# Kernel tuning notes

Measured on AMD Instinct MI355X. Metric: run time of the kernel, lower is better.

## Reference

```python
import jax, jax.numpy as jnp
import numpy as np

N = 1_000_000
NG = 128                 # n_grid
DX = 1.0 / NG
DT = 1e-4
P_VOL = (DX * 0.5) ** 2
P_RHO = 1.0
GRAVITY = 9.8
HID = 16


def setup_inputs() -> dict:
    key = jax.random.key(0)
    ks = jax.random.split(key, 14)
    x = 0.1 + 0.8 * jax.random.uniform(ks[0], (N, 2), dtype=jnp.float32)
    v = 0.1 * jax.random.normal(ks[1], (N, 2), dtype=jnp.float32)
    C = 0.01 * jax.random.normal(ks[2], (N, 2, 2), dtype=jnp.float32)
    F = jnp.eye(2, dtype=jnp.float32)[None] + 0.01 * jax.random.normal(ks[3], (N, 2, 2), dtype=jnp.float32)
    material = jax.random.randint(ks[4], (N,), 0, 3, dtype=jnp.int32)
    Jp = jnp.ones((N, 1), dtype=jnp.float32)
    E = jnp.full((1,), 1000.0, dtype=jnp.float32)
    nu = jnp.full((1,), 0.2, dtype=jnp.float32)
    # PsiModel2d MLP params: Linear(2,16) -> Linear(16,16) -> Linear(16,16) -> Linear(16,1)
    s = 0.3
    W1 = s * jax.random.normal(ks[5], (HID, 2), dtype=jnp.float32)
    b1 = jnp.zeros((HID,), dtype=jnp.float32)
    W2 = s * jax.random.normal(ks[6], (HID, HID), dtype=jnp.float32)
    b2 = jnp.zeros((HID,), dtype=jnp.float32)
    W3 = s * jax.random.normal(ks[7], (HID, HID), dtype=jnp.float32)
    b3 = jnp.zeros((HID,), dtype=jnp.float32)
    W4 = s * jax.random.normal(ks[8], (1, HID), dtype=jnp.float32)
    b4 = jnp.zeros((1,), dtype=jnp.float32)
    return dict(x=x, v=v, C=C, F=F, material=material, Jp=Jp, E=E, nu=nu,
                W1=W1, b1=b1, W2=W2, b2=b2, W3=W3, b3=b3, W4=W4, b4=b4)


def _psi_sum(F, W1, b1, W2, b2, W3, b3, W4, b4):
    # PsiModel2d, input_type='eigen': Psi(sigma_1, sigma_2) of C = F^T F
    Cm = jnp.einsum('nki,nkj->nij', F, F)
    tr_C = Cm[:, 0, 0] + Cm[:, 1, 1]
    det_C = Cm[:, 0, 0] * Cm[:, 1, 1] - Cm[:, 0, 1] * Cm[:, 1, 0]
    delta = jnp.sqrt(jnp.maximum(tr_C ** 2 - 4.0 * det_C, 1e-8))
    feat = jnp.stack([0.5 * (tr_C + delta), 0.5 * (tr_C - delta)], axis=1)  # [N,2]
    h = jax.nn.relu(feat @ W1.T + b1)
    h = jax.nn.relu(h @ W2.T + b2)
    h = jax.nn.relu(h @ W3.T + b3)
    return (h @ W4.T + b4).sum()


def reference(x, v, C, F, material, Jp, E, nu, W1, b1, W2, b2, W3, b3, W4, b4):
    inv_dx = float(NG)
    p_mass = P_VOL * P_RHO
    n = x.shape[0]

    base = jnp.floor(x * inv_dx - 0.5).astype(jnp.int32)   # [N,2]
    fx = x * inv_dx - base.astype(x.dtype)                  # [N,2]
    # quadratic B-spline weights, [3,N,2]
    w = jnp.stack([0.5 * (1.5 - fx) ** 2,
                   0.75 - (fx - 1.0) ** 2,
                   0.5 * (fx - 0.5) ** 2], axis=0)

    F_new = F + DT * jnp.einsum('nij,njk->nik', C, F)
    # stress = d(sum Psi)/dF  (learned energy)
    stress = jax.grad(_psi_sum)(F_new, W1, b1, W2, b2, W3, b3, W4, b4)
    stress = (-DT * P_VOL * 4.0 * inv_dx ** 2) * stress
    affine = stress + p_mass * C                            # [N,2,2]

    v_add = p_mass * v - jnp.einsum('nij,nj->ni', affine, x)  # [N,2]
    vals = jnp.concatenate([v_add, affine.reshape(n, 4),
                            jnp.full((n, 1), p_mass, x.dtype)], axis=1)  # [N,7]

    # P2G: scatter-add over 3x3 stencil into flattened grid
    grid = jnp.zeros((NG * NG, 7), x.dtype)
    for i in range(3):
        for j in range(3):
            wt = w[i, :, 0] * w[j, :, 1]                    # [N]
            idx = (base[:, 0] + i) * NG + (base[:, 1] + j)  # [N]
            grid = grid.at[idx].add(wt[:, None] * vals)
    grid = grid.reshape(NG, NG, 7)
    grid_v = grid[..., :2]
    grid_affine = grid[..., 2:6].reshape(NG, NG, 2, 2)
    grid_m = grid[..., 6]

    gx = jnp.stack(jnp.meshgrid(jnp.arange(NG), jnp.arange(NG), indexing='ij'),
                   axis=-1).astype(x.dtype) * DX            # [NG,NG,2]
    grid_v = grid_v + jnp.einsum('xyij,xyj->xyi', grid_affine, gx)
    nonempty = grid_m > 0
    grid_v = jnp.where(nonempty[..., None],
                       grid_v / jnp.where(nonempty, grid_m, 1.0)[..., None],
                       grid_v)
    grid_v = grid_v.at[:, :, 1].add(-DT * GRAVITY)
    # boundary conditions
    grid_v = grid_v.at[:3, :, 0].set(jnp.maximum(grid_v[:3, :, 0], 0.0))
    grid_v = grid_v.at[-3:, :, 0].set(jnp.minimum(grid_v[-3:, :, 0], 0.0))
    grid_v = grid_v.at[:, :3, 1].set(jnp.maximum(grid_v[:, :3, 1], 0.0))
    grid_v = grid_v.at[:, -3:, 1].set(jnp.minimum(grid_v[:, -3:, 1], 0.0))

    # G2P: gather v and v (x) grid_x outer product over 3x3 stencil
    grid_C = grid_v[..., :, None] * gx[..., None, :]        # [NG,NG,2,2]
    gvals = jnp.concatenate([grid_v, grid_C.reshape(NG, NG, 4)], axis=-1)  # [NG,NG,6]
    acc = jnp.zeros((n, 6), x.dtype)
    for i in range(3):
        for j in range(3):
            wt = w[i, :, 0] * w[j, :, 1]
            acc = acc + wt[:, None] * gvals[base[:, 0] + i, base[:, 1] + j]
    new_v = acc[:, :2]
    new_C = acc[:, 2:].reshape(n, 2, 2)
    new_C = (4.0 * inv_dx ** 2) * (new_C - new_v[:, :, None] * x[:, None, :])

    return (x + DT * v, new_v, new_C, F_new, material, Jp)
```

## Files before the change

### kernel.cpp

```cpp
#include <hip/hip_runtime.h>
#include <math.h>

constexpr int   NGc    = 128;
constexpr int   NCELL  = NGc * NGc;
constexpr int   NBIN   = 128 * 128;
constexpr float DTc    = 1e-4f;
constexpr float DXc    = 1.0f / 128.0f;
constexpr float INV_DX = 128.0f;
constexpr float P_VOLc = (DXc * 0.5f) * (DXc * 0.5f);
constexpr float P_MASSc = P_VOLc * 1.0f;
constexpr float GRAV   = 9.8f;
constexpr float STRESS_COEF = -DTc * P_VOLc * 4.0f * INV_DX * INV_DX;

constexpr int KEY_SHIFT = 18;
constexpr unsigned KEY_MASK = (1u << KEY_SHIFT) - 1u;

constexpr int S1_PPT = 4;
constexpr int S1_BLK = 1024;

__global__ __launch_bounds__(1024) void bin_kernel(
    const float2* __restrict__ x, unsigned* __restrict__ key,
    unsigned* __restrict__ gcnt, int n)
{
    __shared__ unsigned hist[NBIN];
#pragma unroll
    for (int j = 0; j < NBIN / S1_BLK; j++)
        hist[threadIdx.x + j * S1_BLK] = 0;
    __syncthreads();

    int base_i = blockIdx.x * (S1_BLK * S1_PPT);
    unsigned t_arr[S1_PPT], r_arr[S1_PPT];
#pragma unroll
    for (int k = 0; k < S1_PPT; k++) {
        int i = base_i + k * S1_BLK + threadIdx.x;
        unsigned t = 0, r = 0;
        if (i < n) {
            float2 xi = x[i];
            int bx = (int)floorf(xi.x * INV_DX - 0.5f);
            int by = (int)floorf(xi.y * INV_DX - 0.5f);
            t = (unsigned)(bx * 128 + by);
            r = atomicAdd(&hist[t], 1u);
        }
        t_arr[k] = t; r_arr[k] = r;
    }
    __syncthreads();

#pragma unroll
    for (int j = 0; j < NBIN / S1_BLK; j++) {
        int b = threadIdx.x + j * S1_BLK;
        unsigned c = hist[b];
        __syncthreads();
        hist[b] = c ? atomicAdd(&gcnt[b], c) : 0u;
        __syncthreads();
    }

#pragma unroll
    for (int k = 0; k < S1_PPT; k++) {
        int i = base_i + k * S1_BLK + threadIdx.x;
        if (i < n)
            key[i] = (t_arr[k] << KEY_SHIFT) | (hist[t_arr[k]] + r_arr[k]);
    }
}

__global__ __launch_bounds__(1024) void scan_kernel(
    const unsigned* __restrict__ gcnt, unsigned* __restrict__ binoff)
{
    __shared__ unsigned s[1024];
    int t = threadIdx.x;
    unsigned v[16];
    unsigned p = 0;
#pragma unroll
    for (int k = 0; k < 16; k++) { v[k] = gcnt[16 * t + k]; p += v[k]; }
    s[t] = p;
    __syncthreads();
    for (int d = 1; d < 1024; d <<= 1) {
        unsigned add = (t >= d) ? s[t - d] : 0u;
        __syncthreads();
        s[t] += add;
        __syncthreads();
    }
    unsigned base = s[t] - p;
#pragma unroll
    for (int k = 0; k < 16; k++) { binoff[16 * t + k] = base; base += v[k]; }
    if (t == 1023) binoff[NBIN] = s[1023];
}

#define RL(v, l) __int_as_float(__builtin_amdgcn_readlane(__float_as_int(v), (l)))

__global__ __launch_bounds__(256) void stagea_kernel(
    const float2* __restrict__ x, const float2* __restrict__ v,
    const float4* __restrict__ C, const float4* __restrict__ F,
    const float* __restrict__ W1, const float* __restrict__ b1,
    const float* __restrict__ W2, const float* __restrict__ b2,
    const float* __restrict__ W3, const float* __restrict__ b3,
    const float* __restrict__ W4,
    const unsigned* __restrict__ key, const unsigned* __restrict__ binoff,
    float4* __restrict__ recs, float4* __restrict__ out_F, int n)
{
    const int lane = threadIdx.x & 63;

    float w2r[4], w3r[4];
#pragma unroll
    for (int r = 0; r < 4; r++) {
        w2r[r] = W2[r * 64 + lane];
        w3r[r] = W3[r * 64 + lane];
    }
    float wa = (lane < 32) ? W1[lane]
             : ((lane < 48) ? b1[lane - 32] : W4[lane - 48]);
    float wb = (lane < 16) ? b2[lane]
             : ((lane < 32) ? b3[lane - 16] : 0.0f);

    int i = blockIdx.x * 256 + threadIdx.x;
    if (i >= n) return;

    float2 xi = x[i];
    float2 vi = v[i];
    float4 Ci = C[i];
    float4 Fi = F[i];

    float Fn00 = Fi.x + DTc * (Ci.x * Fi.x + Ci.y * Fi.z);
    float Fn01 = Fi.y + DTc * (Ci.x * Fi.y + Ci.y * Fi.w);
    float Fn10 = Fi.z + DTc * (Ci.z * Fi.x + Ci.w * Fi.z);
    float Fn11 = Fi.w + DTc * (Ci.z * Fi.y + Ci.w * Fi.w);

    out_F[i] = make_float4(Fn00, Fn01, Fn10, Fn11);

    float Cm00 = Fn00 * Fn00 + Fn10 * Fn10;
    float Cm01 = Fn00 * Fn01 + Fn10 * Fn11;
    float Cm11 = Fn01 * Fn01 + Fn11 * Fn11;

    float tr  = Cm00 + Cm11;
    float det = Cm00 * Cm11 - Cm01 * Cm01;
    float g   = tr * tr - 4.0f * det;
    float gate = (g > 1e-8f) ? 1.0f : 0.0f;
    float delta = sqrtf(fmaxf(g, 1e-8f));
    float feat0 = 0.5f * (tr + delta);
    float feat1 = 0.5f * (tr - delta);

    float h1[16];
#pragma unroll
    for (int j = 0; j < 16; j++) {
        float a = RL(wa, 2 * j) * feat0 + RL(wa, 2 * j + 1) * feat1 + RL(wa, 32 + j);
        h1[j] = fmaxf(a, 0.0f);
    }

    float h2[16];
#pragma unroll
    for (int j = 0; j < 16; j++) {
        float a0 = RL(wb, j), a1 = 0.0f, a2 = 0.0f, a3 = 0.0f;
#pragma unroll
        for (int k = 0; k < 16; k += 4) {
            a0 += RL(w2r[(16 * j + k + 0) >> 6], (16 * j + k + 0) & 63) * h1[k + 0];
            a1 += RL(w2r[(16 * j + k + 1) >> 6], (16 * j + k + 1) & 63) * h1[k + 1];
            a2 += RL(w2r[(16 * j + k + 2) >> 6], (16 * j + k + 2) & 63) * h1[k + 2];
            a3 += RL(w2r[(16 * j + k + 3) >> 6], (16 * j + k + 3) & 63) * h1[k + 3];
        }
        h2[j] = fmaxf((a0 + a1) + (a2 + a3), 0.0f);
    }

    float dh3[16];
#pragma unroll
    for (int j = 0; j < 16; j++) {
        float a0 = RL(wb, 16 + j), a1 = 0.0f, a2 = 0.0f, a3 = 0.0f;
#pragma unroll
        for (int k = 0; k < 16; k += 4) {
            a0 += RL(w3r[(16 * j + k + 0) >> 6], (16 * j + k + 0) & 63) * h2[k + 0];
            a1 += RL(w3r[(16 * j + k + 1) >> 6], (16 * j + k + 1) & 63) * h2[k + 1];
            a2 += RL(w3r[(16 * j + k + 2) >> 6], (16 * j + k + 2) & 63) * h2[k + 2];
            a3 += RL(w3r[(16 * j + k + 3) >> 6], (16 * j + k + 3) & 63) * h2[k + 3];
        }
        float a = (a0 + a1) + (a2 + a3);
        dh3[j] = (a > 0.0f) ? RL(wa, 48 + j) : 0.0f;
    }

    float dh2[16];
#pragma unroll
    for (int kk = 0; kk < 16; kk++) {
        float a0 = 0.0f, a1 = 0.0f, a2 = 0.0f, a3 = 0.0f;
#pragma unroll
        for (int j = 0; j < 16; j += 4) {
            a0 += RL(w3r[(16 * (j + 0) + kk) >> 6], (16 * (j + 0) + kk) & 63) * dh3[j + 0];
            a1 += RL(w3r[(16 * (j + 1) + kk) >> 6], (16 * (j + 1) + kk) & 63) * dh3[j + 1];
            a2 += RL(w3r[(16 * (j + 2) + kk) >> 6], (16 * (j + 2) + kk) & 63) * dh3[j + 2];
            a3 += RL(w3r[(16 * (j + 3) + kk) >> 6], (16 * (j + 3) + kk) & 63) * dh3[j + 3];
        }
        float a = (a0 + a1) + (a2 + a3);
        dh2[kk] = (h2[kk] > 0.0f) ? a : 0.0f;
    }

    float dfeat0 = 0.0f, dfeat1 = 0.0f;
#pragma unroll
    for (int kk = 0; kk < 16; kk++) {
        float a0 = 0.0f, a1 = 0.0f, a2 = 0.0f, a3 = 0.0f;
#pragma unroll
        for (int j = 0; j < 16; j += 4) {
            a0 += RL(w2r[(16 * (j + 0) + kk) >> 6], (16 * (j + 0) + kk) & 63) * dh2[j + 0];
            a1 += RL(w2r[(16 * (j + 1) + kk) >> 6], (16 * (j + 1) + kk) & 63) * dh2[j + 1];
            a2 += RL(w2r[(16 * (j + 2) + kk) >> 6], (16 * (j + 2) + kk) & 63) * dh2[j + 2];
            a3 += RL(w2r[(16 * (j + 3) + kk) >> 6], (16 * (j + 3) + kk) & 63) * dh2[j + 3];
        }
        float a = (a0 + a1) + (a2 + a3);
        float dh1k = (h1[kk] > 0.0f) ? a : 0.0f;
        dfeat0 += RL(wa, 2 * kk) * dh1k;
        dfeat1 += RL(wa, 2 * kk + 1) * dh1k;
    }

    float half_sum  = 0.5f * (dfeat0 + dfeat1);
    float half_diff = 0.5f * (dfeat0 - dfeat1);
    float inv_delta = 1.0f / delta;
    float dtr  = half_sum + half_diff * tr * inv_delta * gate;
    float ddet = half_diff * (-2.0f) * inv_delta * gate;

    float S00 = 2.0f * (dtr + ddet * Cm11);
    float S11 = 2.0f * (dtr + ddet * Cm00);
    float S01 = -2.0f * ddet * Cm01;

    float dF00 = Fn00 * S00 + Fn01 * S01;
    float dF01 = Fn00 * S01 + Fn01 * S11;
    float dF10 = Fn10 * S00 + Fn11 * S01;
    float dF11 = Fn10 * S01 + Fn11 * S11;

    float a00 = STRESS_COEF * dF00 + P_MASSc * Ci.x;
    float a01 = STRESS_COEF * dF01 + P_MASSc * Ci.y;
    float a10 = STRESS_COEF * dF10 + P_MASSc * Ci.z;
    float a11 = STRESS_COEF * dF11 + P_MASSc * Ci.w;

    unsigned k = key[i];
    unsigned pos = binoff[k >> KEY_SHIFT] + (k & KEY_MASK);

    recs[2 * (size_t)pos]     = make_float4(xi.x, xi.y, a00, a01);
    recs[2 * (size_t)pos + 1] = make_float4(a10, a11, P_MASSc * vi.x, P_MASSc * vi.y);
}

__global__ __launch_bounds__(256) void grid_gather_kernel(
    const float4* __restrict__ recs, const unsigned* __restrict__ binoff,
    float2* __restrict__ gv)
{
    int wid  = threadIdx.x >> 6;
    int lane = threadIdx.x & 63;
    int node = blockIdx.x * 4 + wid;
    int gi = node >> 7;
    int gj = node & 127;

    const float gxx = (float)gi * DXc;
    const float gxy = (float)gj * DXc;

    float accx = 0.0f, accy = 0.0f, accm = 0.0f;

    int j0 = max(gj - 2, 0);

#pragma unroll
    for (int r = 0; r < 3; r++) {
        int bx = gi - 2 + r;
        if (bx < 0 || bx > 127) continue;
        int lo = (int)binoff[bx * 128 + j0];
        int hi = (int)binoff[bx * 128 + gj + 1];
        for (int k = lo + lane; k < hi; k += 64) {
            float4 r0 = recs[2 * (size_t)k];
            float4 r1 = recs[2 * (size_t)k + 1];

            float py = r0.y * INV_DX;
            int   by = (int)floorf(py - 0.5f);
            int   jj = gj - by;

            float fy = py - (float)by;
            float fx = r0.x * INV_DX - (float)bx;

            float wx;
            if (r == 0)      wx = 0.5f * (fx - 0.5f) * (fx - 0.5f);
            else if (r == 1) wx = 0.75f - (fx - 1.0f) * (fx - 1.0f);
            else             wx = 0.5f * (1.5f - fx) * (1.5f - fx);

            float wy0 = 0.5f * (1.5f - fy) * (1.5f - fy);
            float wy1 = 0.75f - (fy - 1.0f) * (fy - 1.0f);
            float wy2 = 0.5f * (fy - 0.5f) * (fy - 0.5f);
            float wy = (jj == 0) ? wy0 : ((jj == 1) ? wy1 : wy2);

            float wt = wx * wy;
            float dxp = gxx - r0.x;
            float dyp = gxy - r0.y;
            accx += wt * (r1.z + r0.z * dxp + r0.w * dyp);
            accy += wt * (r1.w + r1.x * dxp + r1.y * dyp);
            accm += wt * P_MASSc;
        }
    }

#pragma unroll
    for (int off = 32; off >= 1; off >>= 1) {
        accx += __shfl_xor(accx, off, 64);
        accy += __shfl_xor(accy, off, 64);
        accm += __shfl_xor(accm, off, 64);
    }

    if (lane == 0) {
        float vx = accx, vy = accy;
        if (accm > 0.0f) {
            float inv_m = 1.0f / accm;
            vx *= inv_m;
            vy *= inv_m;
        }
        vy -= DTc * GRAV;
        if (gi < 3)        vx = fmaxf(vx, 0.0f);
        if (gi >= NGc - 3) vx = fminf(vx, 0.0f);
        if (gj < 3)        vy = fmaxf(vy, 0.0f);
        if (gj >= NGc - 3) vy = fminf(vy, 0.0f);
        gv[node] = make_float2(vx, vy);
    }
}

__global__ __launch_bounds__(256) void g2p_kernel(
    const float2* __restrict__ x, const float2* __restrict__ v,
    const int* __restrict__ material, const float* __restrict__ Jp,
    const float2* __restrict__ gv,
    float2* __restrict__ out_x, float2* __restrict__ out_v,
    float4* __restrict__ out_C,
    float* __restrict__ out_mat, float* __restrict__ out_Jp, int n)
{
    int i = blockIdx.x * 256 + threadIdx.x;
    if (i >= n) return;

    float2 xi = x[i];
    float2 vi = v[i];

    float px = xi.x * INV_DX, py = xi.y * INV_DX;
    int   bx = (int)floorf(px - 0.5f);
    int   by = (int)floorf(py - 0.5f);
    float fx = px - (float)bx;
    float fy = py - (float)by;
    float wxs[3] = {0.5f * (1.5f - fx) * (1.5f - fx),
                    0.75f - (fx - 1.0f) * (fx - 1.0f),
                    0.5f * (fx - 0.5f) * (fx - 0.5f)};
    float wys[3] = {0.5f * (1.5f - fy) * (1.5f - fy),
                    0.75f - (fy - 1.0f) * (fy - 1.0f),
                    0.5f * (fy - 0.5f) * (fy - 0.5f)};

    float accvx = 0.0f, accvy = 0.0f;
    float accC00 = 0.0f, accC01 = 0.0f, accC10 = 0.0f, accC11 = 0.0f;

#pragma unroll
    for (int ii = 0; ii < 3; ii++) {
        float gxx = (float)(bx + ii) * DXc;
#pragma unroll
        for (int jj = 0; jj < 3; jj++) {
            float wt = wxs[ii] * wys[jj];
            float2 gvn = gv[(bx + ii) * NGc + (by + jj)];
            float gxy = (float)(by + jj) * DXc;
            accvx  += wt * gvn.x;
            accvy  += wt * gvn.y;
            accC00 += wt * gvn.x * gxx;
            accC01 += wt * gvn.x * gxy;
            accC10 += wt * gvn.y * gxx;
            accC11 += wt * gvn.y * gxy;
        }
    }

    const float k4 = 4.0f * INV_DX * INV_DX;
    out_x[i]   = make_float2(xi.x + DTc * vi.x, xi.y + DTc * vi.y);
    out_v[i]   = make_float2(accvx, accvy);
    out_C[i]   = make_float4(k4 * (accC00 - accvx * xi.x),
                             k4 * (accC01 - accvx * xi.y),
                             k4 * (accC10 - accvy * xi.x),
                             k4 * (accC11 - accvy * xi.y));
    out_mat[i] = (float)material[i];
    out_Jp[i]  = Jp[i];
}

extern "C" void kernel_launch(void* const* d_in, const int* in_sizes, int n_in,
                              void* d_out, int out_size, void* d_ws, size_t ws_size,
                              hipStream_t stream)
{
    const float2* x  = (const float2*)d_in[0];
    const float2* v  = (const float2*)d_in[1];
    const float4* C  = (const float4*)d_in[2];
    const float4* F  = (const float4*)d_in[3];
    const int* material = (const int*)d_in[4];
    const float* Jp  = (const float*)d_in[5];
    const float* W1  = (const float*)d_in[8];
    const float* b1  = (const float*)d_in[9];
    const float* W2  = (const float*)d_in[10];
    const float* b2  = (const float*)d_in[11];
    const float* W3  = (const float*)d_in[12];
    const float* b3  = (const float*)d_in[13];
    const float* W4  = (const float*)d_in[14];

    const int n = in_sizes[0] / 2;

    float2* gv = (float2*)d_ws;

    float* out = (float*)d_out;
    float2* out_x   = (float2*)out;
    float2* out_v   = (float2*)(out + 2 * (size_t)n);
    float4* out_C   = (float4*)(out + 4 * (size_t)n);
    float4* out_F   = (float4*)(out + 8 * (size_t)n);
    float*  out_mat = out + 12 * (size_t)n;
    float*  out_Jp  = out + 13 * (size_t)n;

    float4*   recs   = (float4*)out;
    unsigned* key    = (unsigned*)out_mat;
    unsigned* gcnt   = (unsigned*)(out + 13 * (size_t)n);
    unsigned* binoff = gcnt + NBIN;

    hipMemsetAsync(gcnt, 0, NBIN * sizeof(unsigned), stream);

    int s1_blocks = (n + S1_BLK * S1_PPT - 1) / (S1_BLK * S1_PPT);
    int blocks    = (n + 255) / 256;
    bin_kernel<<<s1_blocks, S1_BLK, 0, stream>>>(x, key, gcnt, n);
    scan_kernel<<<1, 1024, 0, stream>>>(gcnt, binoff);
    stagea_kernel<<<blocks, 256, 0, stream>>>(x, v, C, F, W1, b1, W2, b2, W3, b3, W4,
                                              key, binoff, recs, out_F, n);
    grid_gather_kernel<<<NCELL / 4, 256, 0, stream>>>(recs, binoff, gv);
    g2p_kernel<<<blocks, 256, 0, stream>>>(x, v, material, Jp, gv,
                                           out_x, out_v, out_C, out_mat, out_Jp, n);
}
```

Before: 254.0 us.

## Replace global atomic bin offsets with per-block histograms and column scan

The binning kernel now writes each block's local histogram to a per-block count table instead of atomically adding into a global counter array. A new column-scan kernel turns these into per-block exclusive offsets and per-bin totals, and stage A adds the per-block offset when scattering records. Blocks are also made larger, cutting the grid to about 58 blocks, which removes global atomics, the memset and the second key pass. The price is a serial per-bin scan over blocks, an extra kernel launch, another indirect load in stage A, and low occupancy in the binning pass.

```diff
diff --git a/kernel.cpp b/kernel.cpp
--- a/kernel.cpp
+++ b/kernel.cpp
@@ -15,12 +15,13 @@
 constexpr int KEY_SHIFT = 18;
 constexpr unsigned KEY_MASK = (1u << KEY_SHIFT) - 1u;
 
-constexpr int S1_PPT = 4;
-constexpr int S1_BLK = 1024;
+constexpr int S1_PPT   = 17;
+constexpr int S1_BLK   = 1024;
+constexpr int S1_CHUNK = S1_BLK * S1_PPT;
 
 __global__ __launch_bounds__(1024) void bin_kernel(
     const float2* __restrict__ x, unsigned* __restrict__ key,
-    unsigned* __restrict__ gcnt, int n)
+    unsigned* __restrict__ counts, int n)
 {
     __shared__ unsigned hist[NBIN];
 #pragma unroll
@@ -28,49 +29,53 @@
         hist[threadIdx.x + j * S1_BLK] = 0;
     __syncthreads();
 
-    int base_i = blockIdx.x * (S1_BLK * S1_PPT);
-    unsigned t_arr[S1_PPT], r_arr[S1_PPT];
+    int base_i = blockIdx.x * S1_CHUNK;
 #pragma unroll
     for (int k = 0; k < S1_PPT; k++) {
         int i = base_i + k * S1_BLK + threadIdx.x;
-        unsigned t = 0, r = 0;
         if (i < n) {
             float2 xi = x[i];
             int bx = (int)floorf(xi.x * INV_DX - 0.5f);
             int by = (int)floorf(xi.y * INV_DX - 0.5f);
-            t = (unsigned)(bx * 128 + by);
-            r = atomicAdd(&hist[t], 1u);
-        }
-        t_arr[k] = t; r_arr[k] = r;
+            unsigned t = (unsigned)(bx * 128 + by);
+            unsigned r = atomicAdd(&hist[t], 1u);
+            key[i] = (t << KEY_SHIFT) | r;
+        }
     }
     __syncthreads();
 
+    unsigned* row = counts + (size_t)blockIdx.x * NBIN;
 #pragma unroll
     for (int j = 0; j < NBIN / S1_BLK; j++) {
         int b = threadIdx.x + j * S1_BLK;
-        unsigned c = hist[b];
-        __syncthreads();
-        hist[b] = c ? atomicAdd(&gcnt[b], c) : 0u;
-        __syncthreads();
-    }
-
-#pragma unroll
-    for (int k = 0; k < S1_PPT; k++) {
-        int i = base_i + k * S1_BLK + threadIdx.x;
-        if (i < n)
-            key[i] = (t_arr[k] << KEY_SHIFT) | (hist[t_arr[k]] + r_arr[k]);
-    }
+        row[b] = hist[b];
+    }
+}
+
+__global__ __launch_bounds__(256) void scan_blocks_kernel(
+    unsigned* __restrict__ counts, unsigned* __restrict__ bintotal, int nblk)
+{
+    int bin = blockIdx.x * 256 + threadIdx.x;
+    if (bin >= NBIN) return;
+    unsigned run = 0;
+    for (int b = 0; b < nblk; b++) {
+        size_t idx = (size_t)b * NBIN + bin;
+        unsigned c = counts[idx];
+        counts[idx] = run;
+        run += c;
+    }
+    bintotal[bin] = run;
 }
 
 __global__ __launch_bounds__(1024) void scan_kernel(
-    const unsigned* __restrict__ gcnt, unsigned* __restrict__ binoff)
+    const unsigned* __restrict__ bintotal, unsigned* __restrict__ binbase)
 {
     __shared__ unsigned s[1024];
     int t = threadIdx.x;
     unsigned v[16];
     unsigned p = 0;
 #pragma unroll
-    for (int k = 0; k < 16; k++) { v[k] = gcnt[16 * t + k]; p += v[k]; }
+    for (int k = 0; k < 16; k++) { v[k] = bintotal[16 * t + k]; p += v[k]; }
     s[t] = p;
     __syncthreads();
     for (int d = 1; d < 1024; d <<= 1) {
@@ -81,8 +86,8 @@
     }
     unsigned base = s[t] - p;
 #pragma unroll
-    for (int k = 0; k < 16; k++) { binoff[16 * t + k] = base; base += v[k]; }
-    if (t == 1023) binoff[NBIN] = s[1023];
+    for (int k = 0; k < 16; k++) { binbase[16 * t + k] = base; base += v[k]; }
+    if (t == 1023) binbase[NBIN] = s[1023];
 }
 
 #define RL(v, l) __int_as_float(__builtin_amdgcn_readlane(__float_as_int(v), (l)))
@@ -94,7 +99,8 @@
     const float* __restrict__ W2, const float* __restrict__ b2,
     const float* __restrict__ W3, const float* __restrict__ b3,
     const float* __restrict__ W4,
-    const unsigned* __restrict__ key, const unsigned* __restrict__ binoff,
+    const unsigned* __restrict__ key, const unsigned* __restrict__ binbase,
+    const unsigned* __restrict__ counts,
     float4* __restrict__ recs, float4* __restrict__ out_F, int n)
 {
     const int lane = threadIdx.x & 63;
@@ -225,8 +231,10 @@
     float a10 = STRESS_COEF * dF10 + P_MASSc * Ci.z;
     float a11 = STRESS_COEF * dF11 + P_MASSc * Ci.w;
 
-    unsigned k = key[i];
-    unsigned pos = binoff[k >> KEY_SHIFT] + (k & KEY_MASK);
+    unsigned k   = key[i];
+    unsigned bin = k >> KEY_SHIFT;
+    int      blk = i / S1_CHUNK;
+    unsigned pos = binbase[bin] + counts[(size_t)blk * NBIN + bin] + (k & KEY_MASK);
 
     recs[2 * (size_t)pos]     = make_float4(xi.x, xi.y, a00, a01);
     recs[2 * (size_t)pos + 1] = make_float4(a10, a11, P_MASSc * vi.x, P_MASSc * vi.y);
@@ -385,7 +393,9 @@
 
     const int n = in_sizes[0] / 2;
 
-    float2* gv = (float2*)d_ws;
+    float2*   gv       = (float2*)d_ws;
+    unsigned* bintotal = (unsigned*)((char*)d_ws + NCELL * sizeof(float2));
+    unsigned* binbase  = bintotal + NBIN;
 
     float* out = (float*)d_out;
     float2* out_x   = (float2*)out;
@@ -397,18 +407,17 @@
 
     float4*   recs   = (float4*)out;
     unsigned* key    = (unsigned*)out_mat;
-    unsigned* gcnt   = (unsigned*)(out + 13 * (size_t)n);
-    unsigned* binoff = gcnt + NBIN;
-
-    hipMemsetAsync(gcnt, 0, NBIN * sizeof(unsigned), stream);
-
-    int s1_blocks = (n + S1_BLK * S1_PPT - 1) / (S1_BLK * S1_PPT);
+    unsigned* counts = (unsigned*)(out + 13 * (size_t)n);
+
+    int s1_blocks = (n + S1_CHUNK - 1) / S1_CHUNK;
     int blocks    = (n + 255) / 256;
-    bin_kernel<<<s1_blocks, S1_BLK, 0, stream>>>(x, key, gcnt, n);
-    scan_kernel<<<1, 1024, 0, stream>>>(gcnt, binoff);
+
+    bin_kernel<<<s1_blocks, S1_BLK, 0, stream>>>(x, key, counts, n);
+    scan_blocks_kernel<<<(NBIN + 255) / 256, 256, 0, stream>>>(counts, bintotal, s1_blocks);
+    scan_kernel<<<1, 1024, 0, stream>>>(bintotal, binbase);
     stagea_kernel<<<blocks, 256, 0, stream>>>(x, v, C, F, W1, b1, W2, b2, W3, b3, W4,
-                                              key, binoff, recs, out_F, n);
-    grid_gather_kernel<<<NCELL / 4, 256, 0, stream>>>(recs, binoff, gv);
+                                              key, binbase, counts, recs, out_F, n);
+    grid_gather_kernel<<<NCELL / 4, 256, 0, stream>>>(recs, binbase, gv);
     g2p_kernel<<<blocks, 256, 0, stream>>>(x, v, material, Jp, gv,
                                            out_x, out_v, out_C, out_mat, out_Jp, n);
 }
```

After: 268.0 us. +5.5%, slower.
